# Kernel tuning notes

Hardware: AMD Instinct MI355X
Metric: run time of the kernel (lower is better)

Reference implementation:

```python
import jax, jax.numpy as jnp
import numpy as np

N = 100000      # nodes
E = 1600000     # edges (avg degree 16)
F = 128         # feature dim (in == out)
H = 4           # heads
ALPHA = 0.2     # leaky relu slope


def setup_inputs() -> dict:
    key = jax.random.key(0)
    k1, k2, k3, k4, k5 = jax.random.split(key, 5)
    inputs = jax.random.normal(k1, (N, F), dtype=jnp.float32)
    # ensure every node appears as a destination row (src of message) so rowsum > 0
    src = jnp.concatenate([jnp.arange(N, dtype=jnp.int32),
                           jax.random.randint(k2, (E - N,), 0, N, dtype=jnp.int32)])
    dst = jax.random.randint(k3, (E,), 0, N, dtype=jnp.int32)
    edge = jnp.stack([src, dst])  # [2, E], rows = adj.indices()
    adj_values = jax.random.uniform(k4, (E,), dtype=jnp.float32)
    W = jnp.ones((H, F), dtype=jnp.float32)  # nn.init.ones_ per head
    stdv = 1.0 / np.sqrt(2.0 * F)
    a = jax.random.uniform(k5, (H, 2 * F), dtype=jnp.float32, minval=-stdv, maxval=stdv)
    return {"inputs": inputs, "edge": edge, "adj_values": adj_values, "W": W, "a": a}


def reference(inputs, edge, adj_values, W, a):
    src, dst = edge[0], edge[1]
    acc = jnp.zeros_like(inputs)
    for k in range(H):  # small fixed head loop (distinct params per head)
        h = inputs * W[k]                       # [N, F] elementwise scale
        # a.mm([h_src; h_dst]) decomposes into per-node partial scores
        s_src = h @ a[k, :F]                    # [N]
        s_dst = h @ a[k, F:]                    # [N]
        e = jnp.exp(jax.nn.leaky_relu(s_src[src] + s_dst[dst], ALPHA)) * adj_values  # [E]
        rowsum = jax.ops.segment_sum(e, src, num_segments=N)               # [N]
        h_prime = jax.ops.segment_sum(e[:, None] * h[dst], src, num_segments=N)  # [N, F]
        acc = acc + jax.nn.elu(h_prime / rowsum[:, None])  # concat=True -> elu
    return acc / H  # mean over heads
```

## Files before the change

kernel.cpp:

```cpp
#include <hip/hip_runtime.h>

#define FDIM   128
#define HEADS  4
#define ALPHA  0.2f
#define DMASK  0x03FFFFFF
#define PT     4096
#define NBMAX  1568

typedef float v2f __attribute__((ext_vector_type(2)));

__device__ __forceinline__ float readlane_f(float v, int lane) {
  return __int_as_float(__builtin_amdgcn_readlane(__float_as_int(v), lane));
}

__global__ __launch_bounds__(256) void score_kernel(
    const float* __restrict__ x, const float* __restrict__ W,
    const float* __restrict__ a, float* __restrict__ s_src,
    float* __restrict__ s_dst, unsigned int* __restrict__ xb,
    const int* __restrict__ src, int* __restrict__ hist,
    int E, int HB, int n) {
  __shared__ int h[NBMAX];
  int lane = threadIdx.x & 63;
  int node = (blockIdx.x << 2) + (threadIdx.x >> 6);
  if (node < n) {
    const float2* x2 = (const float2*)x;
    const float2* W2 = (const float2*)W;
    const float2* a2 = (const float2*)a;
    float2 xv = x2[(size_t)node * 64 + lane];

    unsigned int u0 = __float_as_uint(xv.x);
    unsigned int u1 = __float_as_uint(xv.y);
    u0 += 0x7fffu + ((u0 >> 16) & 1u);
    u1 += 0x7fffu + ((u1 >> 16) & 1u);
    xb[(size_t)node * 64 + lane] = (u0 >> 16) | (u1 & 0xffff0000u);

    float p[8];
#pragma unroll
    for (int k = 0; k < HEADS; k++) {
      float2 wv = W2[k * 64 + lane];
      float hx = xv.x * wv.x, hy = xv.y * wv.y;
      float2 as_ = a2[k * 128 + lane];
      float2 ad_ = a2[k * 128 + 64 + lane];
      p[k]         = hx * as_.x + hy * as_.y;
      p[4 + k]     = hx * ad_.x + hy * ad_.y;
    }

    bool h5 = (lane & 32) != 0;
    float q[4];
#pragma unroll
    for (int k = 0; k < 4; k++) {
      float send = h5 ? p[k] : p[4 + k];
      float got = __shfl_xor(send, 32);
      q[k] = (h5 ? p[4 + k] : p[k]) + got;
    }
    bool h4 = (lane & 16) != 0;
    float r[2];
#pragma unroll
    for (int j = 0; j < 2; j++) {
      float send = h4 ? q[j] : q[2 + j];
      float got = __shfl_xor(send, 16);
      r[j] = (h4 ? q[2 + j] : q[j]) + got;
    }
    bool h3 = (lane & 8) != 0;
    float send = h3 ? r[0] : r[1];
    float got = __shfl_xor(send, 8);
    float v = (h3 ? r[1] : r[0]) + got;
    v += __shfl_xor(v, 1);
    v += __shfl_xor(v, 2);
    v += __shfl_xor(v, 4);
    if ((lane & 7) == 0) {
      int s = lane >> 3;
      if (s < 4) s_src[node * HEADS + s] = v;
      else       s_dst[node * HEADS + (s - 4)] = v;
    }
  }

  int b = blockIdx.x;
  if (b < HB) {
    int t = threadIdx.x;
    int NB = (n + 63) >> 6;
    for (int i = t; i < NB; i += 256) h[i] = 0;
    __syncthreads();
    int base = b * 8192;
#pragma unroll 4
    for (int j = 0; j < 32; j++) {
      int i = base + j * 256 + t;
      if (i < E) atomicAdd(&h[src[i] >> 6], 1);
    }
    __syncthreads();
    for (int i = t; i < NB; i += 256)
      if (h[i]) atomicAdd(&hist[i], h[i]);
  }
}

__global__ __launch_bounds__(256) void scan_kernel(const int* __restrict__ hist,
                                                   int* __restrict__ fine_ptr,
                                                   int* __restrict__ cursor,
                                                   int NB, int E) {
  __shared__ int lds[256];
  int t = threadIdx.x;
  int loc[8];
  int s = 0;
#pragma unroll
  for (int j = 0; j < 8; j++) {
    int idx = t * 8 + j;
    loc[j] = (idx < NB) ? hist[idx] : 0;
    s += loc[j];
  }
  lds[t] = s;
  __syncthreads();
  for (int off = 1; off < 256; off <<= 1) {
    int xv = (t >= off) ? lds[t - off] : 0;
    __syncthreads();
    lds[t] += xv;
    __syncthreads();
  }
  int run = lds[t] - s;
#pragma unroll
  for (int j = 0; j < 8; j++) {
    int idx = t * 8 + j;
    if (idx < NB) {
      fine_ptr[idx] = run;
      cursor[idx]   = run;
    }
    run += loc[j];
  }
  if (t == 0) fine_ptr[NB] = E;
}

__global__ __launch_bounds__(256) void partition_kernel(
    const int* __restrict__ src, const int* __restrict__ dst,
    const float* __restrict__ adj, int* __restrict__ cursor,
    int2* __restrict__ ebuf, int E, int NB) {
  __shared__ int h[NBMAX];
  __shared__ int sc[NBMAX];
  __shared__ int bg[NBMAX];
  __shared__ unsigned short keyarr[PT];
  __shared__ int2 es[PT];
  __shared__ int lds[256];

  int t = threadIdx.x;
  int base = blockIdx.x * PT;
  for (int i = t; i < NB; i += 256) h[i] = 0;
  __syncthreads();

  int ssrc[16];
#pragma unroll
  for (int j = 0; j < 16; j++) {
    int i = base + j * 256 + t;
    ssrc[j] = (i < E) ? src[i] : -1;
    if (ssrc[j] >= 0) atomicAdd(&h[ssrc[j] >> 6], 1);
  }
  __syncthreads();

  int loc[8];
  int s = 0;
#pragma unroll
  for (int j = 0; j < 8; j++) {
    int idx = t * 8 + j;
    loc[j] = (idx < NB) ? h[idx] : 0;
    s += loc[j];
  }
  lds[t] = s;
  __syncthreads();
  for (int off = 1; off < 256; off <<= 1) {
    int xv = (t >= off) ? lds[t - off] : 0;
    __syncthreads();
    lds[t] += xv;
    __syncthreads();
  }
  int run = lds[t] - s;
#pragma unroll
  for (int j = 0; j < 8; j++) {
    int idx = t * 8 + j;
    if (idx < NB) sc[idx] = run;
    run += loc[j];
  }
  __syncthreads();

  for (int i = t; i < NB; i += 256)
    if (h[i]) bg[i] = atomicAdd(&cursor[i], h[i]);
  __syncthreads();

#pragma unroll
  for (int j = 0; j < 16; j++) {
    if (ssrc[j] >= 0) {
      int i = base + j * 256 + t;
      int k = ssrc[j] >> 6;
      int slot = atomicAdd(&sc[k], 1);
      int2 pk;
      pk.x = (int)(((unsigned)(ssrc[j] & 63) << 26) | (unsigned)dst[i]);
      pk.y = __float_as_int(adj[i]);
      es[slot] = pk;
      keyarr[slot] = (unsigned short)k;
    }
  }
  __syncthreads();

  int tc = E - base; if (tc > PT) tc = PT;
  for (int s2 = t; s2 < tc; s2 += 256) {
    int k = keyarr[s2];
    int rank = s2 - (sc[k] - h[k]);
    ebuf[bg[k] + rank] = es[s2];
  }
}

__global__ __launch_bounds__(256, 8) void aggregate_kernel(
    const unsigned int* __restrict__ xb, const float* __restrict__ W,
    const float* __restrict__ s_src, const float* __restrict__ s_dst,
    const int* __restrict__ fine_ptr, const int2* __restrict__ ebuf,
    float* __restrict__ out, int n) {
  __shared__ int2  es[512];
  __shared__ float evbuf[4][64];
  __shared__ int   nbeg[17];
  __shared__ int   nrun[16];
  __shared__ int   h[16];

  int t = threadIdx.x, bb = blockIdx.x;
  int b0 = bb >> 2, qtr = bb & 3;
  int lane = t & 63, wid = t >> 6;
  int beg = fine_ptr[b0];
  int L   = fine_ptr[b0 + 1] - beg;

  if (t < 16) h[t] = 0;
  __syncthreads();
  for (int i = t; i < L; i += 256) {
    int kk = (unsigned)ebuf[beg + i].x >> 26;
    if ((kk >> 4) == qtr) atomicAdd(&h[kk & 15], 1);
  }
  __syncthreads();
  if (t < 16) {
    int v = h[t];
#pragma unroll
    for (int off = 1; off < 16; off <<= 1) {
      int u = __shfl_up(v, off);
      if (lane >= off) v += u;
    }
    nbeg[t + 1] = v;
    nrun[t] = v - h[t];
    if (t == 0) nbeg[0] = 0;
  }
  __syncthreads();
  for (int i = t; i < L; i += 256) {
    int2 pk = ebuf[beg + i];
    int kk = (unsigned)pk.x >> 26;
    if ((kk >> 4) == qtr) {
      int slot = atomicAdd(&nrun[kk & 15], 1);
      es[slot] = pk;
    }
  }
  __syncthreads();

  int e = lane >> 2;
  int k = lane & 3;

  for (int ni = 0; ni < 4; ni++) {
    int nl = wid * 4 + ni;
    int node = (b0 << 6) + (qtr << 4) + nl;
    if (node >= n) break;
    int eb = nbeg[nl], cnt = nbeg[nl + 1] - eb;
    float ssrc_k = s_src[node * HEADS + k];

    v2f acc0{0.f,0.f}, acc1{0.f,0.f}, acc2{0.f,0.f}, acc3{0.f,0.f};
    float rsum = 0.f;

    int c = 0;
    while (c < cnt) {
      int cn = cnt - c; if (cn > 16) cn = 16;
      int2 pk{0, 0};
      if (e < cn) pk = es[eb + c + e];
      int dv = pk.x & DMASK;

      float sdv = s_dst[dv * HEADS + k];
      int dd[16];
#pragma unroll
      for (int j = 0; j < 16; j++)
        dd[j] = __builtin_amdgcn_readlane(pk.x, j * 4) & DMASK;
      unsigned int xw[16];
#pragma unroll
      for (int j = 0; j < 16; j++)
        xw[j] = xb[((unsigned)dd[j] << 6) + lane];

      float s = ssrc_k + sdv;
      s = (s >= 0.f) ? s : ALPHA * s;
      float ev = __expf(s) * __int_as_float(pk.y);
      rsum += ev;
      evbuf[wid][lane] = ev;

#pragma unroll
      for (int j = 0; j < 16; j++) {
        const float4 s4 = *(const float4*)&evbuf[wid][j * 4];
        v2f xv;
        xv.x = __uint_as_float(xw[j] << 16);
        xv.y = __uint_as_float(xw[j] & 0xffff0000u);
        acc0 += s4.x * xv;
        acc1 += s4.y * xv;
        acc2 += s4.z * xv;
        acc3 += s4.w * xv;
      }
      c += 16;
    }

    rsum += __shfl_xor(rsum, 4);
    rsum += __shfl_xor(rsum, 8);
    rsum += __shfl_xor(rsum, 16);
    rsum += __shfl_xor(rsum, 32);
    float rinv = __builtin_amdgcn_rcpf(rsum);
    float r0 = readlane_f(rinv, 0), r1 = readlane_f(rinv, 1);
    float r2 = readlane_f(rinv, 2), r3 = readlane_f(rinv, 3);

    const float2* W2 = (const float2*)W;
    float2 o{0.f, 0.f};
    float hx, hy;
    {
      float2 wv = W2[0 * 64 + lane];
      hx = wv.x * acc0.x * r0; hy = wv.y * acc0.y * r0;
      o.x += (hx > 0.f) ? hx : (__expf(hx) - 1.f);
      o.y += (hy > 0.f) ? hy : (__expf(hy) - 1.f);
    }
    {
      float2 wv = W2[1 * 64 + lane];
      hx = wv.x * acc1.x * r1; hy = wv.y * acc1.y * r1;
      o.x += (hx > 0.f) ? hx : (__expf(hx) - 1.f);
      o.y += (hy > 0.f) ? hy : (__expf(hy) - 1.f);
    }
    {
      float2 wv = W2[2 * 64 + lane];
      hx = wv.x * acc2.x * r2; hy = wv.y * acc2.y * r2;
      o.x += (hx > 0.f) ? hx : (__expf(hx) - 1.f);
      o.y += (hy > 0.f) ? hy : (__expf(hy) - 1.f);
    }
    {
      float2 wv = W2[3 * 64 + lane];
      hx = wv.x * acc3.x * r3; hy = wv.y * acc3.y * r3;
      o.x += (hx > 0.f) ? hx : (__expf(hx) - 1.f);
      o.y += (hy > 0.f) ? hy : (__expf(hy) - 1.f);
    }
    o.x *= 0.25f; o.y *= 0.25f;
    ((float2*)out)[(size_t)node * 64 + lane] = o;
  }
}

extern "C" void kernel_launch(void* const* d_in, const int* in_sizes, int n_in,
                              void* d_out, int out_size, void* d_ws, size_t ws_size,
                              hipStream_t stream) {
  const float* x   = (const float*)d_in[0];
  const int*   edg = (const int*)d_in[1];
  const float* adj = (const float*)d_in[2];
  const float* W   = (const float*)d_in[3];
  const float* a   = (const float*)d_in[4];
  float* out = (float*)d_out;

  int E = in_sizes[2];
  int n = in_sizes[0] / FDIM;
  const int* src = edg;
  const int* dst = edg + E;
  int NB = (n + 63) >> 6;
  int HB = (E + 8191) / 8192;

  auto align = [](size_t v) { return (v + 255) & ~(size_t)255; };
  char* ws = (char*)d_ws;
  int*   fine_ptr = (int*)ws;          ws += align((size_t)(NB + 1) * 4);
  int*   cursor   = (int*)ws;          ws += align((size_t)NB * 4);
  int*   hist     = (int*)ws;          ws += align((size_t)NB * 4);
  int2*  ebuf     = (int2*)ws;         ws += align((size_t)E * 8);
  float* s_src    = (float*)ws;        ws += align((size_t)n * HEADS * 4);
  float* s_dst    = (float*)ws;        ws += align((size_t)n * HEADS * 4);
  unsigned int* xb = (unsigned int*)ws; ws += align((size_t)n * 64 * 4);

  hipMemsetAsync(hist, 0, (size_t)NB * 4, stream);

  score_kernel<<<(n + 3) / 4, 256, 0, stream>>>(x, W, a, s_src, s_dst, xb,
                                                src, hist, E, HB, n);
  scan_kernel<<<1, 256, 0, stream>>>(hist, fine_ptr, cursor, NB, E);
  partition_kernel<<<(E + PT - 1) / PT, 256, 0, stream>>>(src, dst, adj, cursor,
                                                          ebuf, E, NB);
  aggregate_kernel<<<NB * 4, 256, 0, stream>>>(xb, W, s_src, s_dst, fine_ptr,
                                               ebuf, out, n);
}
```

Measured before the change: 280.2 us.

## Recast aggregation as bf16 MFMA with split-precision weights and LDS gather

The per-node scalar FMA aggregation loop is replaced by a per-wave scheme. Each wave gathers 32 neighbor bf16 rows straight into LDS with global_load_lds, then builds a masked 16x32 weight matrix (4 nodes x 4 heads per row) split into hi and lo bf16 parts. MFMA 16x16x32 instructions accumulate the features, and a ones-vector MFMA computes the row sums. This aims to move the gather-multiply-accumulate onto matrix cores and to batch the neighbor loads, but it doubles the MFMA work for precision and lowers occupancy to 4 blocks per CU because of the larger LDS footprint.

```diff
diff --git a/kernel.cpp b/kernel.cpp
--- a/kernel.cpp
+++ b/kernel.cpp
@@ -8,10 +8,9 @@
 #define NBMAX  1568
 
 typedef float v2f __attribute__((ext_vector_type(2)));
-
-__device__ __forceinline__ float readlane_f(float v, int lane) {
-  return __int_as_float(__builtin_amdgcn_readlane(__float_as_int(v), lane));
-}
+typedef __attribute__((ext_vector_type(8))) short bf16x8;
+typedef __attribute__((ext_vector_type(4))) float f32x4;
+typedef __attribute__((ext_vector_type(4))) unsigned u32x4;
 
 __global__ __launch_bounds__(256) void score_kernel(
     const float* __restrict__ x, const float* __restrict__ W,
@@ -41,8 +40,8 @@
       float hx = xv.x * wv.x, hy = xv.y * wv.y;
       float2 as_ = a2[k * 128 + lane];
       float2 ad_ = a2[k * 128 + 64 + lane];
-      p[k]         = hx * as_.x + hy * as_.y;
-      p[4 + k]     = hx * ad_.x + hy * ad_.y;
+      p[k]     = hx * as_.x + hy * as_.y;
+      p[4 + k] = hx * ad_.x + hy * ad_.y;
     }
 
     bool h5 = (lane & 32) != 0;
@@ -205,13 +204,15 @@
   }
 }
 
-__global__ __launch_bounds__(256, 8) void aggregate_kernel(
+__global__ __launch_bounds__(256, 4) void aggregate_kernel(
     const unsigned int* __restrict__ xb, const float* __restrict__ W,
     const float* __restrict__ s_src, const float* __restrict__ s_dst,
     const int* __restrict__ fine_ptr, const int2* __restrict__ ebuf,
     float* __restrict__ out, int n) {
   __shared__ int2  es[512];
-  __shared__ float evbuf[4][64];
+  __shared__ unsigned short xrow[4][32][128];
+  __shared__ float evls[4][192];
+  __shared__ int   own_w[4][32];
   __shared__ int   nbeg[17];
   __shared__ int   nrun[16];
   __shared__ int   h[16];
@@ -251,93 +252,120 @@
   }
   __syncthreads();
 
-  int e = lane >> 2;
-  int k = lane & 3;
-
-  for (int ni = 0; ni < 4; ni++) {
-    int nl = wid * 4 + ni;
-    int node = (b0 << 6) + (qtr << 4) + nl;
-    if (node >= n) break;
-    int eb = nbeg[nl], cnt = nbeg[nl + 1] - eb;
-    float ssrc_k = s_src[node * HEADS + k];
-
-    v2f acc0{0.f,0.f}, acc1{0.f,0.f}, acc2{0.f,0.f}, acc3{0.f,0.f};
-    float rsum = 0.f;
-
-    int c = 0;
-    while (c < cnt) {
-      int cn = cnt - c; if (cn > 16) cn = 16;
-      int2 pk{0, 0};
-      if (e < cn) pk = es[eb + c + e];
-      int dv = pk.x & DMASK;
-
-      float sdv = s_dst[dv * HEADS + k];
-      int dd[16];
-#pragma unroll
-      for (int j = 0; j < 16; j++)
-        dd[j] = __builtin_amdgcn_readlane(pk.x, j * 4) & DMASK;
-      unsigned int xw[16];
-#pragma unroll
-      for (int j = 0; j < 16; j++)
-        xw[j] = xb[((unsigned)dd[j] << 6) + lane];
-
-      float s = ssrc_k + sdv;
-      s = (s >= 0.f) ? s : ALPHA * s;
-      float ev = __expf(s) * __int_as_float(pk.y);
-      rsum += ev;
-      evbuf[wid][lane] = ev;
-
-#pragma unroll
-      for (int j = 0; j < 16; j++) {
-        const float4 s4 = *(const float4*)&evbuf[wid][j * 4];
-        v2f xv;
-        xv.x = __uint_as_float(xw[j] << 16);
-        xv.y = __uint_as_float(xw[j] & 0xffff0000u);
-        acc0 += s4.x * xv;
-        acc1 += s4.y * xv;
-        acc2 += s4.z * xv;
-        acc3 += s4.w * xv;
-      }
-      c += 16;
-    }
-
-    rsum += __shfl_xor(rsum, 4);
-    rsum += __shfl_xor(rsum, 8);
-    rsum += __shfl_xor(rsum, 16);
-    rsum += __shfl_xor(rsum, 32);
-    float rinv = __builtin_amdgcn_rcpf(rsum);
-    float r0 = readlane_f(rinv, 0), r1 = readlane_f(rinv, 1);
-    float r2 = readlane_f(rinv, 2), r3 = readlane_f(rinv, 3);
-
-    const float2* W2 = (const float2*)W;
-    float2 o{0.f, 0.f};
-    float hx, hy;
-    {
-      float2 wv = W2[0 * 64 + lane];
-      hx = wv.x * acc0.x * r0; hy = wv.y * acc0.y * r0;
-      o.x += (hx > 0.f) ? hx : (__expf(hx) - 1.f);
-      o.y += (hy > 0.f) ? hy : (__expf(hy) - 1.f);
-    }
-    {
-      float2 wv = W2[1 * 64 + lane];
-      hx = wv.x * acc1.x * r1; hy = wv.y * acc1.y * r1;
-      o.x += (hx > 0.f) ? hx : (__expf(hx) - 1.f);
-      o.y += (hy > 0.f) ? hy : (__expf(hy) - 1.f);
-    }
-    {
-      float2 wv = W2[2 * 64 + lane];
-      hx = wv.x * acc2.x * r2; hy = wv.y * acc2.y * r2;
-      o.x += (hx > 0.f) ? hx : (__expf(hx) - 1.f);
-      o.y += (hy > 0.f) ? hy : (__expf(hy) - 1.f);
-    }
-    {
-      float2 wv = W2[3 * 64 + lane];
-      hx = wv.x * acc3.x * r3; hy = wv.y * acc3.y * r3;
-      o.x += (hx > 0.f) ? hx : (__expf(hx) - 1.f);
-      o.y += (hy > 0.f) ? hy : (__expf(hy) - 1.f);
-    }
-    o.x *= 0.25f; o.y *= 0.25f;
-    ((float2*)out)[(size_t)node * 64 + lane] = o;
+  int el = lane & 31;
+  int hp = lane >> 5;
+  int kb = (lane >> 4) << 3;
+  int ha = lane & 3;
+  int na = (lane & 15) >> 2;
+  unsigned dsel = (lane & 1) ? 0x07060302u : 0x05040100u;
+
+  bf16x8 bones;
+#pragma unroll
+  for (int j = 0; j < 8; j++) bones[j] = (short)0x3F80;
+
+  f32x4 acc[8];
+#pragma unroll
+  for (int c = 0; c < 8; c++) acc[c] = (f32x4){0.f, 0.f, 0.f, 0.f};
+  f32x4 accR = (f32x4){0.f, 0.f, 0.f, 0.f};
+
+  int wbase = nbeg[wid * 4];
+  int wend  = nbeg[wid * 4 + 4];
+  int gb = (b0 << 6) + (qtr << 4) + wid * 4;
+
+  for (int cb = wbase; cb < wend; cb += 32) {
+    int rem = wend - cb;
+    int2 pk{0, 0};
+    if (el < rem) pk = es[cb + el];
+
+    asm volatile("s_waitcnt lgkmcnt(0)" ::: "memory");
+#pragma unroll
+    for (int j = 0; j < 32; j++) {
+      int dd = __builtin_amdgcn_readlane(pk.x, j) & DMASK;
+      __builtin_amdgcn_global_load_lds(
+          (const __attribute__((address_space(1))) unsigned int*)
+              (xb + (((size_t)(unsigned)dd) << 6) + lane),
+          (__attribute__((address_space(3))) unsigned int*)(&xrow[wid][j][0]),
+          4, 0, 0);
+    }
+
+    unsigned kk = (unsigned)pk.x >> 26;
+    int own_e = (int)(kk & 3);
+    int dv = pk.x & DMASK;
+    int ng = (b0 << 6) + (qtr << 4) + (int)(kk & 15);
+    float2 sv  = *(const float2*)&s_src[ng * 4 + 2 * hp];
+    float2 dvv = *(const float2*)&s_dst[dv * 4 + 2 * hp];
+    float adjv = __int_as_float(pk.y);
+    float s0 = sv.x + dvv.x; s0 = (s0 >= 0.f) ? s0 : ALPHA * s0;
+    float s1 = sv.y + dvv.y; s1 = (s1 >= 0.f) ? s1 : ALPHA * s1;
+    float e0 = __expf(s0) * adjv;
+    float e1 = __expf(s1) * adjv;
+    if (el >= rem) { e0 = 0.f; e1 = 0.f; }
+    *(float2*)&evls[wid][el * 6 + 2 * hp] = float2{e0, e1};
+    own_w[wid][el] = own_e;
+
+    unsigned hw0, hw1, hw2, hw3, lw0, lw1, lw2, lw3;
+#define ABUILD(JP, HW, LW) {                                          \
+      int k0 = kb + 2 * (JP), k1 = k0 + 1;                            \
+      float m0 = evls[wid][k0 * 6 + ha];                              \
+      float m1 = evls[wid][k1 * 6 + ha];                              \
+      m0 = (own_w[wid][k0] == na) ? m0 : 0.f;                         \
+      m1 = (own_w[wid][k1] == na) ? m1 : 0.f;                         \
+      unsigned u0 = __float_as_uint(m0), u1 = __float_as_uint(m1);    \
+      unsigned r0 = u0 + 0x7fffu + ((u0 >> 16) & 1u);                 \
+      unsigned r1 = u1 + 0x7fffu + ((u1 >> 16) & 1u);                 \
+      HW = __builtin_amdgcn_perm(r1, r0, 0x07060302u);                \
+      float l0 = m0 - __uint_as_float(r0 & 0xffff0000u);              \
+      float l1 = m1 - __uint_as_float(r1 & 0xffff0000u);              \
+      LW = __builtin_amdgcn_perm(__float_as_uint(l1),                 \
+                                 __float_as_uint(l0), 0x07060302u); }
+    ABUILD(0, hw0, lw0)
+    ABUILD(1, hw1, lw1)
+    ABUILD(2, hw2, lw2)
+    ABUILD(3, hw3, lw3)
+#undef ABUILD
+    bf16x8 ahi = __builtin_bit_cast(bf16x8, (u32x4){hw0, hw1, hw2, hw3});
+    bf16x8 alo = __builtin_bit_cast(bf16x8, (u32x4){lw0, lw1, lw2, lw3});
+
+    asm volatile("s_waitcnt vmcnt(0)" ::: "memory");
+    int fb = lane & 14;
+#pragma unroll
+    for (int cc = 0; cc < 8; cc++) {
+      unsigned dw[8];
+#pragma unroll
+      for (int j = 0; j < 8; j++)
+        dw[j] = *(const unsigned*)&xrow[wid][kb + j][cc * 16 + fb];
+      u32x4 bw = { __builtin_amdgcn_perm(dw[1], dw[0], dsel),
+                   __builtin_amdgcn_perm(dw[3], dw[2], dsel),
+                   __builtin_amdgcn_perm(dw[5], dw[4], dsel),
+                   __builtin_amdgcn_perm(dw[7], dw[6], dsel) };
+      bf16x8 bfrag = __builtin_bit_cast(bf16x8, bw);
+      acc[cc] = __builtin_amdgcn_mfma_f32_16x16x32_bf16(ahi, bfrag, acc[cc], 0, 0, 0);
+      acc[cc] = __builtin_amdgcn_mfma_f32_16x16x32_bf16(alo, bfrag, acc[cc], 0, 0, 0);
+    }
+    accR = __builtin_amdgcn_mfma_f32_16x16x32_bf16(ahi, bones, accR, 0, 0, 0);
+    accR = __builtin_amdgcn_mfma_f32_16x16x32_bf16(alo, bones, accR, 0, 0, 0);
+  }
+
+  float rinv0 = __builtin_amdgcn_rcpf(accR[0]);
+  float rinv1 = __builtin_amdgcn_rcpf(accR[1]);
+  float rinv2 = __builtin_amdgcn_rcpf(accR[2]);
+  float rinv3 = __builtin_amdgcn_rcpf(accR[3]);
+  int ng4 = gb + (lane >> 4);
+  bool valid = ng4 < n;
+  int fl = lane & 15;
+#pragma unroll
+  for (int cc = 0; cc < 8; cc++) {
+    int f = cc * 16 + fl;
+    float o = 0.f;
+    float v0 = acc[cc][0] * W[0 * 128 + f] * rinv0;
+    o += (v0 > 0.f) ? v0 : (__expf(v0) - 1.f);
+    float v1 = acc[cc][1] * W[1 * 128 + f] * rinv1;
+    o += (v1 > 0.f) ? v1 : (__expf(v1) - 1.f);
+    float v2 = acc[cc][2] * W[2 * 128 + f] * rinv2;
+    o += (v2 > 0.f) ? v2 : (__expf(v2) - 1.f);
+    float v3 = acc[cc][3] * W[3 * 128 + f] * rinv3;
+    o += (v3 > 0.f) ? v3 : (__expf(v3) - 1.f);
+    if (valid) out[(size_t)ng4 * 128 + f] = o * 0.25f;
   }
 }
 
```

Measured after the change: 287.4 us. +2.6%, slower.

## Replace coarse 64-node bucket partition with per-node CSR via global atomics

Applied to the files above, without the earlier changes.

The two-level bucketing (64-node buckets built with LDS histograms, then per-block re-sorting into nodes inside aggregate) is replaced by a full per-node CSR. Histograms now use global atomics per source node, a single-block scan walks all n entries in tiles, and scatter uses a global atomic cursor per node. Aggregate reads per-node offsets directly and prefetches the next 16-edge packet. This removes the LDS resort and extra ebuf passes from aggregate, but adds many contended global atomics and a long serial scan over 100k entries in one block.

```diff
diff --git a/kernel.cpp b/kernel.cpp
--- a/kernel.cpp
+++ b/kernel.cpp
@@ -3,9 +3,6 @@
 #define FDIM   128
 #define HEADS  4
 #define ALPHA  0.2f
-#define DMASK  0x03FFFFFF
-#define PT     4096
-#define NBMAX  1568
 
 typedef float v2f __attribute__((ext_vector_type(2)));
 
@@ -19,7 +16,6 @@
     float* __restrict__ s_dst, unsigned int* __restrict__ xb,
     const int* __restrict__ src, int* __restrict__ hist,
     int E, int HB, int n) {
-  __shared__ int h[NBMAX];
   int lane = threadIdx.x & 63;
   int node = (blockIdx.x << 2) + (threadIdx.x >> 6);
   if (node < n) {
@@ -41,8 +37,8 @@
       float hx = xv.x * wv.x, hy = xv.y * wv.y;
       float2 as_ = a2[k * 128 + lane];
       float2 ad_ = a2[k * 128 + 64 + lane];
-      p[k]         = hx * as_.x + hy * as_.y;
-      p[4 + k]     = hx * ad_.x + hy * ad_.y;
+      p[k]     = hx * as_.x + hy * as_.y;
+      p[4 + k] = hx * ad_.x + hy * ad_.y;
     }
 
     bool h5 = (lane & 32) != 0;
@@ -78,130 +74,74 @@
   int b = blockIdx.x;
   if (b < HB) {
     int t = threadIdx.x;
-    int NB = (n + 63) >> 6;
-    for (int i = t; i < NB; i += 256) h[i] = 0;
-    __syncthreads();
     int base = b * 8192;
 #pragma unroll 4
     for (int j = 0; j < 32; j++) {
       int i = base + j * 256 + t;
-      if (i < E) atomicAdd(&h[src[i] >> 6], 1);
-    }
-    __syncthreads();
-    for (int i = t; i < NB; i += 256)
-      if (h[i]) atomicAdd(&hist[i], h[i]);
+      if (i < E) atomicAdd(&hist[src[i]], 1);
+    }
   }
 }
 
 __global__ __launch_bounds__(256) void scan_kernel(const int* __restrict__ hist,
                                                    int* __restrict__ fine_ptr,
                                                    int* __restrict__ cursor,
-                                                   int NB, int E) {
+                                                   int n, int E) {
   __shared__ int lds[256];
   int t = threadIdx.x;
-  int loc[8];
-  int s = 0;
-#pragma unroll
-  for (int j = 0; j < 8; j++) {
-    int idx = t * 8 + j;
-    loc[j] = (idx < NB) ? hist[idx] : 0;
-    s += loc[j];
-  }
-  lds[t] = s;
-  __syncthreads();
-  for (int off = 1; off < 256; off <<= 1) {
-    int xv = (t >= off) ? lds[t - off] : 0;
+  int carry = 0;
+  int NT = (n + 2047) >> 11;
+  for (int tile = 0; tile < NT; tile++) {
+    int base = tile << 11;
+    int loc[8];
+    int s = 0;
+#pragma unroll
+    for (int j = 0; j < 8; j++) {
+      int idx = base + t * 8 + j;
+      loc[j] = (idx < n) ? hist[idx] : 0;
+      s += loc[j];
+    }
+    lds[t] = s;
     __syncthreads();
-    lds[t] += xv;
+    for (int off = 1; off < 256; off <<= 1) {
+      int xv = (t >= off) ? lds[t - off] : 0;
+      __syncthreads();
+      lds[t] += xv;
+      __syncthreads();
+    }
+    int run = carry + lds[t] - s;
+#pragma unroll
+    for (int j = 0; j < 8; j++) {
+      int idx = base + t * 8 + j;
+      if (idx < n) {
+        fine_ptr[idx] = run;
+        cursor[idx]   = run;
+      }
+      run += loc[j];
+    }
+    carry += lds[255];
     __syncthreads();
   }
-  int run = lds[t] - s;
-#pragma unroll
-  for (int j = 0; j < 8; j++) {
-    int idx = t * 8 + j;
-    if (idx < NB) {
-      fine_ptr[idx] = run;
-      cursor[idx]   = run;
-    }
-    run += loc[j];
-  }
-  if (t == 0) fine_ptr[NB] = E;
-}
-
-__global__ __launch_bounds__(256) void partition_kernel(
+  if (t == 0) fine_ptr[n] = E;
+}
+
+__global__ __launch_bounds__(256) void scatter_kernel(
     const int* __restrict__ src, const int* __restrict__ dst,
     const float* __restrict__ adj, int* __restrict__ cursor,
-    int2* __restrict__ ebuf, int E, int NB) {
-  __shared__ int h[NBMAX];
-  __shared__ int sc[NBMAX];
-  __shared__ int bg[NBMAX];
-  __shared__ unsigned short keyarr[PT];
-  __shared__ int2 es[PT];
-  __shared__ int lds[256];
-
+    int2* __restrict__ ebuf, int E) {
   int t = threadIdx.x;
-  int base = blockIdx.x * PT;
-  for (int i = t; i < NB; i += 256) h[i] = 0;
-  __syncthreads();
-
-  int ssrc[16];
-#pragma unroll
-  for (int j = 0; j < 16; j++) {
+  int base = blockIdx.x * 8192;
+#pragma unroll 4
+  for (int j = 0; j < 32; j++) {
     int i = base + j * 256 + t;
-    ssrc[j] = (i < E) ? src[i] : -1;
-    if (ssrc[j] >= 0) atomicAdd(&h[ssrc[j] >> 6], 1);
-  }
-  __syncthreads();
-
-  int loc[8];
-  int s = 0;
-#pragma unroll
-  for (int j = 0; j < 8; j++) {
-    int idx = t * 8 + j;
-    loc[j] = (idx < NB) ? h[idx] : 0;
-    s += loc[j];
-  }
-  lds[t] = s;
-  __syncthreads();
-  for (int off = 1; off < 256; off <<= 1) {
-    int xv = (t >= off) ? lds[t - off] : 0;
-    __syncthreads();
-    lds[t] += xv;
-    __syncthreads();
-  }
-  int run = lds[t] - s;
-#pragma unroll
-  for (int j = 0; j < 8; j++) {
-    int idx = t * 8 + j;
-    if (idx < NB) sc[idx] = run;
-    run += loc[j];
-  }
-  __syncthreads();
-
-  for (int i = t; i < NB; i += 256)
-    if (h[i]) bg[i] = atomicAdd(&cursor[i], h[i]);
-  __syncthreads();
-
-#pragma unroll
-  for (int j = 0; j < 16; j++) {
-    if (ssrc[j] >= 0) {
-      int i = base + j * 256 + t;
-      int k = ssrc[j] >> 6;
-      int slot = atomicAdd(&sc[k], 1);
+    if (i < E) {
+      int s = src[i];
+      int slot = atomicAdd(&cursor[s], 1);
       int2 pk;
-      pk.x = (int)(((unsigned)(ssrc[j] & 63) << 26) | (unsigned)dst[i]);
+      pk.x = dst[i];
       pk.y = __float_as_int(adj[i]);
-      es[slot] = pk;
-      keyarr[slot] = (unsigned short)k;
-    }
-  }
-  __syncthreads();
-
-  int tc = E - base; if (tc > PT) tc = PT;
-  for (int s2 = t; s2 < tc; s2 += 256) {
-    int k = keyarr[s2];
-    int rank = s2 - (sc[k] - h[k]);
-    ebuf[bg[k] + rank] = es[s2];
+      ebuf[slot] = pk;
+    }
   }
 }
 
@@ -210,80 +150,45 @@
     const float* __restrict__ s_src, const float* __restrict__ s_dst,
     const int* __restrict__ fine_ptr, const int2* __restrict__ ebuf,
     float* __restrict__ out, int n) {
-  __shared__ int2  es[512];
   __shared__ float evbuf[4][64];
-  __shared__ int   nbeg[17];
-  __shared__ int   nrun[16];
-  __shared__ int   h[16];
-
-  int t = threadIdx.x, bb = blockIdx.x;
-  int b0 = bb >> 2, qtr = bb & 3;
+
+  int t = threadIdx.x, b = blockIdx.x;
   int lane = t & 63, wid = t >> 6;
-  int beg = fine_ptr[b0];
-  int L   = fine_ptr[b0 + 1] - beg;
-
-  if (t < 16) h[t] = 0;
-  __syncthreads();
-  for (int i = t; i < L; i += 256) {
-    int kk = (unsigned)ebuf[beg + i].x >> 26;
-    if ((kk >> 4) == qtr) atomicAdd(&h[kk & 15], 1);
-  }
-  __syncthreads();
-  if (t < 16) {
-    int v = h[t];
-#pragma unroll
-    for (int off = 1; off < 16; off <<= 1) {
-      int u = __shfl_up(v, off);
-      if (lane >= off) v += u;
-    }
-    nbeg[t + 1] = v;
-    nrun[t] = v - h[t];
-    if (t == 0) nbeg[0] = 0;
-  }
-  __syncthreads();
-  for (int i = t; i < L; i += 256) {
-    int2 pk = ebuf[beg + i];
-    int kk = (unsigned)pk.x >> 26;
-    if ((kk >> 4) == qtr) {
-      int slot = atomicAdd(&nrun[kk & 15], 1);
-      es[slot] = pk;
-    }
-  }
-  __syncthreads();
-
   int e = lane >> 2;
   int k = lane & 3;
 
   for (int ni = 0; ni < 4; ni++) {
-    int nl = wid * 4 + ni;
-    int node = (b0 << 6) + (qtr << 4) + nl;
+    int node = (b << 4) + wid * 4 + ni;
     if (node >= n) break;
-    int eb = nbeg[nl], cnt = nbeg[nl + 1] - eb;
+    int eb = fine_ptr[node];
+    int cnt = fine_ptr[node + 1] - eb;
     float ssrc_k = s_src[node * HEADS + k];
 
     v2f acc0{0.f,0.f}, acc1{0.f,0.f}, acc2{0.f,0.f}, acc3{0.f,0.f};
     float rsum = 0.f;
 
+    int2 pkC{0, 0};
+    if (e < cnt) pkC = ebuf[eb + e];
+
     int c = 0;
     while (c < cnt) {
-      int cn = cnt - c; if (cn > 16) cn = 16;
-      int2 pk{0, 0};
-      if (e < cn) pk = es[eb + c + e];
-      int dv = pk.x & DMASK;
-
-      float sdv = s_dst[dv * HEADS + k];
+      int2 pkN{0, 0};
+      int cn2 = cnt - c - 16;
+      if (cn2 > 0 && e < cn2) pkN = ebuf[eb + c + 16 + e];
+
+      float sdv = s_dst[pkC.x * HEADS + k];
       int dd[16];
 #pragma unroll
       for (int j = 0; j < 16; j++)
-        dd[j] = __builtin_amdgcn_readlane(pk.x, j * 4) & DMASK;
+        dd[j] = __builtin_amdgcn_readlane(pkC.x, j * 4);
       unsigned int xw[16];
 #pragma unroll
       for (int j = 0; j < 16; j++)
-        xw[j] = xb[((unsigned)dd[j] << 6) + lane];
+        xw[j] = xb[(((size_t)(unsigned)dd[j]) << 6) + lane];
 
       float s = ssrc_k + sdv;
       s = (s >= 0.f) ? s : ALPHA * s;
-      float ev = __expf(s) * __int_as_float(pk.y);
+      float ev = __expf(s) * __int_as_float(pkC.y);
       rsum += ev;
       evbuf[wid][lane] = ev;
 
@@ -298,6 +203,7 @@
         acc2 += s4.z * xv;
         acc3 += s4.w * xv;
       }
+      pkC = pkN;
       c += 16;
     }
 
@@ -355,26 +261,24 @@
   int n = in_sizes[0] / FDIM;
   const int* src = edg;
   const int* dst = edg + E;
-  int NB = (n + 63) >> 6;
   int HB = (E + 8191) / 8192;
 
   auto align = [](size_t v) { return (v + 255) & ~(size_t)255; };
   char* ws = (char*)d_ws;
-  int*   fine_ptr = (int*)ws;          ws += align((size_t)(NB + 1) * 4);
-  int*   cursor   = (int*)ws;          ws += align((size_t)NB * 4);
-  int*   hist     = (int*)ws;          ws += align((size_t)NB * 4);
+  int*   fine_ptr = (int*)ws;          ws += align((size_t)(n + 1) * 4);
+  int*   cursor   = (int*)ws;          ws += align((size_t)n * 4);
+  int*   hist     = (int*)ws;          ws += align((size_t)n * 4);
   int2*  ebuf     = (int2*)ws;         ws += align((size_t)E * 8);
   float* s_src    = (float*)ws;        ws += align((size_t)n * HEADS * 4);
   float* s_dst    = (float*)ws;        ws += align((size_t)n * HEADS * 4);
   unsigned int* xb = (unsigned int*)ws; ws += align((size_t)n * 64 * 4);
 
-  hipMemsetAsync(hist, 0, (size_t)NB * 4, stream);
+  hipMemsetAsync(hist, 0, (size_t)n * 4, stream);
 
   score_kernel<<<(n + 3) / 4, 256, 0, stream>>>(x, W, a, s_src, s_dst, xb,
                                                 src, hist, E, HB, n);
-  scan_kernel<<<1, 256, 0, stream>>>(hist, fine_ptr, cursor, NB, E);
-  partition_kernel<<<(E + PT - 1) / PT, 256, 0, stream>>>(src, dst, adj, cursor,
-                                                          ebuf, E, NB);
-  aggregate_kernel<<<NB * 4, 256, 0, stream>>>(xb, W, s_src, s_dst, fine_ptr,
-                                               ebuf, out, n);
-}
+  scan_kernel<<<1, 256, 0, stream>>>(hist, fine_ptr, cursor, n, E);
+  scatter_kernel<<<HB, 256, 0, stream>>>(src, dst, adj, cursor, ebuf, E);
+  aggregate_kernel<<<(n + 15) / 16, 256, 0, stream>>>(xb, W, s_src, s_dst,
+                                                      fine_ptr, ebuf, out, n);
+}
```

Measured after the change: 535.4 us. +91.1%, slower.
